# Kernel tuning notes

Measured on AMD Instinct MI355X. Metric: run time of the kernel, lower is better.

Reference implementation:

```python
import jax, jax.numpy as jnp
import numpy as np

T, B, E, H = 2048, 4, 1024, 16
HD = E // H
SCALE = HD ** -0.5


def setup_inputs() -> dict:
    key = jax.random.key(0)
    k1, k2, k3 = jax.random.split(key, 3)
    # xavier-ish scaling on weights for numerical sanity
    inputs = jax.random.normal(k1, (T, B, E), dtype=jnp.float32)
    in_proj_weight = jax.random.normal(k2, (3 * E, E), dtype=jnp.float32) * (2.0 / (4 * E)) ** 0.5
    out_proj_weight = jax.random.normal(k3, (E, E), dtype=jnp.float32) * (1.0 / E) ** 0.5
    return {"inputs": inputs, "in_proj_weight": in_proj_weight, "out_proj_weight": out_proj_weight}


def reference(inputs, in_proj_weight, out_proj_weight):
    t, b, e = inputs.shape
    # fused QKV projection: [T,B,E] @ [E,3E] -> [T, B*H, 3, HD]
    qkv = jnp.einsum('tbe,fe->tbf', inputs, in_proj_weight)
    qkv = qkv.reshape(t, b * H, 3, HD)
    q, k, v = qkv[:, :, 0, :], qkv[:, :, 1, :], qkv[:, :, 2, :]  # [T, B*H, HD]
    # scaled attention scores per (batch*head): [B*H, T, T]
    scores = SCALE * jnp.einsum('tnd,snd->nts', q, k)
    probs = jax.nn.softmax(scores, axis=-1)
    # dropout p=0.0 -> identity
    ctx = jnp.einsum('nts,snd->tnd', probs, v).reshape(t, b, e)
    # output projection (applied to attention context, matching intended math / backward)
    return jnp.einsum('tbe,oe->tbo', ctx, out_proj_weight)
```

## Files before the change

### kernel.cpp

```cpp
#include <hip/hip_runtime.h>
#include <stdint.h>
#include <stddef.h>


typedef __attribute__((ext_vector_type(8))) short bf16x8;
typedef __attribute__((ext_vector_type(4))) float f32x4;
typedef __attribute__((ext_vector_type(4))) unsigned int u32x4;

#define MFMA16(a, b, c) __builtin_amdgcn_mfma_f32_16x16x32_bf16((a), (b), (c), 0, 0, 0)

__device__ __forceinline__ unsigned short f2bf(float f) {
  unsigned u = __builtin_bit_cast(unsigned, f);
  u += 0x7fffu + ((u >> 16) & 1u);
  return (unsigned short)(u >> 16);
}

__device__ __forceinline__ float fast_exp2(float x) {
#if __has_builtin(__builtin_amdgcn_exp2f)
  return __builtin_amdgcn_exp2f(x);
#else
  return exp2f(x);
#endif
}

__device__ __forceinline__ unsigned cvtpk(float lo, float hi) {
  unsigned r;
  asm volatile("v_cvt_pk_bf16_f32 %0, %1, %2" : "=v"(r) : "v"(lo), "v"(hi));
  return r;
}

__device__ __forceinline__ void lane_swap32(unsigned &a, unsigned &b) {
#if __has_builtin(__builtin_amdgcn_permlane32_swap)
  auto r = __builtin_amdgcn_permlane32_swap(a, b, false, false);
  a = r[0]; b = r[1];
#else
  const bool hi = (threadIdx.x & 32) != 0;
  unsigned sa = (unsigned)__shfl_xor((int)a, 32, 64);
  unsigned sb = (unsigned)__shfl_xor((int)b, 32, 64);
  unsigned na = hi ? sb : a;
  unsigned nb = hi ? b : sa;
  a = na; b = nb;
#endif
}

__device__ __forceinline__ void lane_swap16(unsigned &a, unsigned &b) {
  const bool odd = (threadIdx.x & 16) != 0;
  unsigned sa = (unsigned)__shfl_xor((int)a, 16, 64);
  unsigned sb = (unsigned)__shfl_xor((int)b, 16, 64);
  unsigned na = odd ? sb : a;
  unsigned nb = odd ? b : sa;
  a = na; b = nb;
}

__device__ __forceinline__ void gload_lds16(const void* g, void* l) {
  __builtin_amdgcn_global_load_lds((const __attribute__((address_space(1))) void*)g,
                                   (__attribute__((address_space(3))) void*)l,
                                   16, 0, 0);
}

__global__ __launch_bounds__(256) void k_cvt(const float* __restrict__ src,
                                             unsigned short* __restrict__ dst, int n4) {
  int i = blockIdx.x * 256 + threadIdx.x;
  if (i >= n4) return;
  const float4 v = ((const float4*)src)[i];
  ushort4 o;
  o.x = f2bf(v.x); o.y = f2bf(v.y); o.z = f2bf(v.z); o.w = f2bf(v.w);
  ((ushort4*)dst)[i] = o;
}

__global__ __launch_bounds__(256, 2) void k_gemm_qkv(
    const unsigned short* __restrict__ A,
    const unsigned short* __restrict__ Bt,
    unsigned short* __restrict__ Qb,
    unsigned short* __restrict__ Kb,
    unsigned short* __restrict__ VTb) {
  constexpr int K = 1024;
  __shared__ __align__(16) unsigned short As[128 * 32];
  __shared__ __align__(16) unsigned short Bs[128 * 32];
  const int tid = threadIdx.x;
  const int l = tid & 63, w = tid >> 6;
  const int lr = l & 15, lg = l >> 4;
  const int bm = blockIdx.x, bn = blockIdx.y;
  const int wr = (w >> 1) * 64, wc = (w & 1) * 64;

  f32x4 acc[4][4] = {};

  const int o0 = tid * 16, o1 = tid * 16 + 4096;
  const int r0 = o0 >> 6, c0 = o0 & 63;
  const int r1 = o1 >> 6, c1 = o1 & 63;
  const char* gA0 = (const char*)A + (size_t)(bm * 128 + r0) * (K * 2) + c0;
  const char* gA1 = (const char*)A + (size_t)(bm * 128 + r1) * (K * 2) + c1;
  const char* gB0 = (const char*)Bt + (size_t)(bn * 128 + r0) * (K * 2) + c0;
  const char* gB1 = (const char*)Bt + (size_t)(bn * 128 + r1) * (K * 2) + c1;
  char* lA0 = (char*)As + o0;
  char* lA1 = (char*)As + o1;
  char* lB0 = (char*)Bs + o0;
  char* lB1 = (char*)Bs + o1;

  for (int kt = 0; kt < K / 32; ++kt) {
    const int kb = kt * 64;
    gload_lds16(gA0 + kb, lA0);
    gload_lds16(gA1 + kb, lA1);
    gload_lds16(gB0 + kb, lB0);
    gload_lds16(gB1 + kb, lB1);
    __syncthreads();
    bf16x8 af[4], bfr[4];
#pragma unroll
    for (int mf = 0; mf < 4; ++mf)
      af[mf] = *(const bf16x8*)&As[(wr + mf * 16 + lr) * 32 + lg * 8];
#pragma unroll
    for (int nf = 0; nf < 4; ++nf)
      bfr[nf] = *(const bf16x8*)&Bs[(wc + nf * 16 + lr) * 32 + lg * 8];
#pragma unroll
    for (int mf = 0; mf < 4; ++mf)
#pragma unroll
      for (int nf = 0; nf < 4; ++nf)
        acc[mf][nf] = MFMA16(af[mf], bfr[nf], acc[mf][nf]);
    __syncthreads();
  }

#pragma unroll
  for (int nf = 0; nf < 4; ++nf) {
    const int f = bn * 128 + wc + nf * 16 + lr;
    const int hq = f / 192;
    const int s3 = (f >> 6) % 3;
    const int d = f & 63;
    const float qscale = (s3 == 0) ? 0.18033688011112042f : 1.0f;
#pragma unroll
    for (int mf = 0; mf < 4; ++mf) {
#pragma unroll
      for (int i = 0; i < 4; ++i) {
        const int r = bm * 128 + wr + mf * 16 + lg * 4 + i;
        const int t = r >> 2, bb2 = r & 3;
        const int nIdx = bb2 * 16 + hq;
        const unsigned short val = f2bf(acc[mf][nf][i] * qscale);
        if (s3 == 0)      Qb[((size_t)nIdx * 2048 + t) * 64 + d] = val;
        else if (s3 == 1) Kb[((size_t)nIdx * 2048 + t) * 64 + d] = val;
        else              VTb[((size_t)nIdx * 64 + d) * 2048 + t] = val;
      }
    }
  }
}

__global__ __launch_bounds__(256, 2) void k_attn(
    const unsigned short* __restrict__ Qb, const unsigned short* __restrict__ Kb,
    const unsigned short* __restrict__ VTb, unsigned short* __restrict__ Cx) {
  __shared__ __align__(16) unsigned short Ks[64 * 64];
  __shared__ __align__(16) unsigned short Vt[64 * 64];

  const int tid = threadIdx.x;
  const int l = tid & 63, w = tid >> 6;
  const int lq = l & 15, lg = l >> 4;
  const int qt = blockIdx.x, n = blockIdx.y;

  const unsigned short* Qh = Qb + (size_t)n * (2048 * 64);
  const unsigned short* Kh = Kb + (size_t)n * (2048 * 64);
  const unsigned short* Vh = VTb + (size_t)n * (64 * 2048);

  bf16x8 aq[2][2];
#pragma unroll
  for (int qf = 0; qf < 2; ++qf)
#pragma unroll
    for (int kd = 0; kd < 2; ++kd)
      aq[qf][kd] = *(const bf16x8*)&Qh[(size_t)(qt * 128 + w * 32 + qf * 16 + lq) * 64 +
                                       kd * 32 + lg * 8];

  f32x4 o[4][2] = {};
  float lsum[2] = {0.f, 0.f};

#pragma unroll 1
  for (int st = 0; st < 32; ++st) {
    const int s0 = st * 64;
#pragma unroll
    for (int it = 0; it < 2; ++it) {
      const int off = (it * 256 + tid) * 16;
      const int row = off >> 7;
      const int colb = (off & 127) ^ ((row & 7) << 4);
      gload_lds16((const char*)Kh + (size_t)(s0 + row) * 128 + colb, (char*)Ks + off);
      gload_lds16((const char*)Vh + (size_t)row * 4096 + s0 * 2 + colb, (char*)Vt + off);
    }
    __syncthreads();

    f32x4 sc[2][4];
#pragma unroll
    for (int sf = 0; sf < 4; ++sf) {
      const int rowk = sf * 16 + lq;
      const int sw = (rowk & 7) << 4;
      bf16x8 k0 = *(const bf16x8*)((const char*)Ks + ((rowk * 128 + lg * 16) ^ sw));
      bf16x8 k1 = *(const bf16x8*)((const char*)Ks + ((rowk * 128 + 64 + lg * 16) ^ sw));
#pragma unroll
      for (int qf = 0; qf < 2; ++qf) {
        f32x4 z = {0.f, 0.f, 0.f, 0.f};
        z = MFMA16(k0, aq[qf][0], z);
        z = MFMA16(k1, aq[qf][1], z);
        sc[qf][sf] = z;
      }
    }

#pragma unroll
    for (int qf = 0; qf < 2; ++qf) {
      float accs = 0.f;
#pragma unroll
      for (int sf = 0; sf < 4; ++sf)
#pragma unroll
        for (int i = 0; i < 4; ++i) {
          const float p = fast_exp2(sc[qf][sf][i]);
          sc[qf][sf][i] = p;
          accs += p;
        }
      lsum[qf] += accs;
    }

#pragma unroll
    for (int kb = 0; kb < 2; ++kb) {
      bf16x8 pf[2];
#pragma unroll
      for (int qf = 0; qf < 2; ++qf) {
        unsigned w0 = cvtpk(sc[qf][2 * kb + 0][0], sc[qf][2 * kb + 0][1]);
        unsigned w1 = cvtpk(sc[qf][2 * kb + 0][2], sc[qf][2 * kb + 0][3]);
        unsigned w2 = cvtpk(sc[qf][2 * kb + 1][0], sc[qf][2 * kb + 1][1]);
        unsigned w3 = cvtpk(sc[qf][2 * kb + 1][2], sc[qf][2 * kb + 1][3]);
        lane_swap32(w0, w2);
        lane_swap32(w1, w3);
        lane_swap16(w0, w2);
        lane_swap16(w1, w3);
        u32x4 t4 = {w0, w1, w2, w3};
        pf[qf] = __builtin_bit_cast(bf16x8, t4);
      }
#pragma unroll
      for (int df = 0; df < 4; ++df) {
        const int rowd = df * 16 + lq;
        const int sw = (rowd & 7) << 4;
        bf16x8 vf = *(const bf16x8*)((const char*)Vt + ((rowd * 128 + kb * 64 + lg * 16) ^ sw));
#pragma unroll
        for (int qf = 0; qf < 2; ++qf)
          o[df][qf] = MFMA16(vf, pf[qf], o[df][qf]);
      }
    }
    __syncthreads();
  }

  const int bb = n >> 4, h = n & 15;
#pragma unroll
  for (int qf = 0; qf < 2; ++qf) {
    float li = lsum[qf];
    li += __shfl_xor(li, 16, 64);
    li += __shfl_xor(li, 32, 64);
    const float inv = 1.0f / li;
    const int q = qt * 128 + w * 32 + qf * 16 + lq;
#pragma unroll
    for (int df = 0; df < 4; ++df) {
      ushort4 pk;
      pk.x = f2bf(o[df][qf][0] * inv);
      pk.y = f2bf(o[df][qf][1] * inv);
      pk.z = f2bf(o[df][qf][2] * inv);
      pk.w = f2bf(o[df][qf][3] * inv);
      *(ushort4*)&Cx[(size_t)(q * 4 + bb) * 1024 + h * 64 + df * 16 + lg * 4] = pk;
    }
  }
}

__global__ __launch_bounds__(256, 2) void k_gemm_out(
    const unsigned short* __restrict__ A,
    const unsigned short* __restrict__ Bt,
    float* __restrict__ C) {
  constexpr int K = 1024;
  __shared__ __align__(16) unsigned short As[128 * 32];
  __shared__ __align__(16) unsigned short Bs[128 * 32];
  const int tid = threadIdx.x;
  const int l = tid & 63, w = tid >> 6;
  const int lr = l & 15, lg = l >> 4;
  const int bm = blockIdx.x, bn = blockIdx.y;
  const int wr = (w >> 1) * 64, wc = (w & 1) * 64;

  f32x4 acc[4][4] = {};

  const int o0 = tid * 16, o1 = tid * 16 + 4096;
  const int r0 = o0 >> 6, c0 = o0 & 63;
  const int r1 = o1 >> 6, c1 = o1 & 63;
  const char* gA0 = (const char*)A + (size_t)(bm * 128 + r0) * (K * 2) + c0;
  const char* gA1 = (const char*)A + (size_t)(bm * 128 + r1) * (K * 2) + c1;
  const char* gB0 = (const char*)Bt + (size_t)(bn * 128 + r0) * (K * 2) + c0;
  const char* gB1 = (const char*)Bt + (size_t)(bn * 128 + r1) * (K * 2) + c1;
  char* lA0 = (char*)As + o0;
  char* lA1 = (char*)As + o1;
  char* lB0 = (char*)Bs + o0;
  char* lB1 = (char*)Bs + o1;

  for (int kt = 0; kt < K / 32; ++kt) {
    const int kb = kt * 64;
    gload_lds16(gA0 + kb, lA0);
    gload_lds16(gA1 + kb, lA1);
    gload_lds16(gB0 + kb, lB0);
    gload_lds16(gB1 + kb, lB1);
    __syncthreads();
    bf16x8 af[4], bfr[4];
#pragma unroll
    for (int mf = 0; mf < 4; ++mf)
      af[mf] = *(const bf16x8*)&As[(wr + mf * 16 + lr) * 32 + lg * 8];
#pragma unroll
    for (int nf = 0; nf < 4; ++nf)
      bfr[nf] = *(const bf16x8*)&Bs[(wc + nf * 16 + lr) * 32 + lg * 8];
#pragma unroll
    for (int mf = 0; mf < 4; ++mf)
#pragma unroll
      for (int nf = 0; nf < 4; ++nf)
        acc[mf][nf] = MFMA16(af[mf], bfr[nf], acc[mf][nf]);
    __syncthreads();
  }

#pragma unroll
  for (int mf = 0; mf < 4; ++mf)
#pragma unroll
    for (int i = 0; i < 4; ++i) {
      const int r = bm * 128 + wr + mf * 16 + lg * 4 + i;
#pragma unroll
      for (int nf = 0; nf < 4; ++nf)
        C[(size_t)r * 1024 + bn * 128 + wc + nf * 16 + lr] = acc[mf][nf][i];
    }
}

extern "C" void kernel_launch(void* const* d_in, const int* in_sizes, int n_in,
                              void* d_out, int out_size, void* d_ws, size_t ws_size,
                              hipStream_t stream) {
  const float* X = (const float*)d_in[0];
  const float* W1 = (const float*)d_in[1];
  const float* Wo = (const float*)d_in[2];
  float* out = (float*)d_out;

  char* ws = (char*)d_ws;
  unsigned short* Xb  = (unsigned short*)(ws);
  unsigned short* W1b = (unsigned short*)(ws + 16777216);
  unsigned short* Wob = (unsigned short*)(ws + 23068672);
  unsigned short* Qb  = (unsigned short*)(ws + 25165824);
  unsigned short* Kb  = (unsigned short*)(ws + 41943040);
  unsigned short* VTb = (unsigned short*)(ws + 58720256);
  unsigned short* Cx  = (unsigned short*)(ws + 75497472);

  k_cvt<<<8192, 256, 0, stream>>>(X, Xb, 2097152);
  k_cvt<<<3072, 256, 0, stream>>>(W1, W1b, 786432);
  k_cvt<<<1024, 256, 0, stream>>>(Wo, Wob, 262144);
  k_gemm_qkv<<<dim3(64, 24), 256, 0, stream>>>(Xb, W1b, Qb, Kb, VTb);
  k_attn<<<dim3(16, 64), 256, 0, stream>>>(Qb, Kb, VTb, Cx);
  k_gemm_out<<<dim3(64, 8), 256, 0, stream>>>(Cx, Wob, out);
}
```

Measured before the change: 213.2 us.

## Double-buffer attention K/V tiles, add V transpose kernel, use K16 MFMA for PV

Attention now double-buffers the K and V^T LDS tiles, prefetching the next tile while computing the current one, and uses explicit waitcnt and barrier with s_setprio around the MFMA sections. The QKV GEMM writes V in row layout and a new transpose kernel builds V^T, replacing the strided scatter stores. The PV product uses 16x16x16 MFMA when available, which removes the lane-swap permutes. The attention grid is reordered so that blocks sharing a head are adjacent. This adds one kernel launch and an extra V round trip through memory, and it reuses the Cx buffer region for Vb.

```diff
diff --git a/kernel.cpp b/kernel.cpp
--- a/kernel.cpp
+++ b/kernel.cpp
@@ -4,10 +4,17 @@
 
 
 typedef __attribute__((ext_vector_type(8))) short bf16x8;
+typedef __attribute__((ext_vector_type(4))) short bf16x4;
 typedef __attribute__((ext_vector_type(4))) float f32x4;
 typedef __attribute__((ext_vector_type(4))) unsigned int u32x4;
+typedef __attribute__((ext_vector_type(2))) unsigned int u32x2;
 
 #define MFMA16(a, b, c) __builtin_amdgcn_mfma_f32_16x16x32_bf16((a), (b), (c), 0, 0, 0)
+
+#if __has_builtin(__builtin_amdgcn_mfma_f32_16x16x16bf16_1k)
+#define HAVE_K16 1
+#define MFMAK16(a, b, c) __builtin_amdgcn_mfma_f32_16x16x16bf16_1k((a), (b), (c), 0, 0, 0)
+#endif
 
 __device__ __forceinline__ unsigned short f2bf(float f) {
   unsigned u = __builtin_bit_cast(unsigned, f);
@@ -29,6 +36,7 @@
   return r;
 }
 
+#ifndef HAVE_K16
 __device__ __forceinline__ void lane_swap32(unsigned &a, unsigned &b) {
 #if __has_builtin(__builtin_amdgcn_permlane32_swap)
   auto r = __builtin_amdgcn_permlane32_swap(a, b, false, false);
@@ -42,7 +50,6 @@
   a = na; b = nb;
 #endif
 }
-
 __device__ __forceinline__ void lane_swap16(unsigned &a, unsigned &b) {
   const bool odd = (threadIdx.x & 16) != 0;
   unsigned sa = (unsigned)__shfl_xor((int)a, 16, 64);
@@ -51,6 +58,7 @@
   unsigned nb = odd ? b : sa;
   a = na; b = nb;
 }
+#endif
 
 __device__ __forceinline__ void gload_lds16(const void* g, void* l) {
   __builtin_amdgcn_global_load_lds((const __attribute__((address_space(1))) void*)g,
@@ -73,7 +81,7 @@
     const unsigned short* __restrict__ Bt,
     unsigned short* __restrict__ Qb,
     unsigned short* __restrict__ Kb,
-    unsigned short* __restrict__ VTb) {
+    unsigned short* __restrict__ Vb) {
   constexpr int K = 1024;
   __shared__ __align__(16) unsigned short As[128 * 32];
   __shared__ __align__(16) unsigned short Bs[128 * 32];
@@ -125,6 +133,7 @@
     const int hq = f / 192;
     const int s3 = (f >> 6) % 3;
     const int d = f & 63;
+    unsigned short* dst = (s3 == 0) ? Qb : (s3 == 1) ? Kb : Vb;
     const float qscale = (s3 == 0) ? 0.18033688011112042f : 1.0f;
 #pragma unroll
     for (int mf = 0; mf < 4; ++mf) {
@@ -133,25 +142,47 @@
         const int r = bm * 128 + wr + mf * 16 + lg * 4 + i;
         const int t = r >> 2, bb2 = r & 3;
         const int nIdx = bb2 * 16 + hq;
-        const unsigned short val = f2bf(acc[mf][nf][i] * qscale);
-        if (s3 == 0)      Qb[((size_t)nIdx * 2048 + t) * 64 + d] = val;
-        else if (s3 == 1) Kb[((size_t)nIdx * 2048 + t) * 64 + d] = val;
-        else              VTb[((size_t)nIdx * 64 + d) * 2048 + t] = val;
+        dst[((size_t)nIdx * 2048 + t) * 64 + d] = f2bf(acc[mf][nf][i] * qscale);
       }
     }
   }
+}
+
+__global__ __launch_bounds__(256) void k_vtrans(const unsigned short* __restrict__ V,
+                                                unsigned short* __restrict__ VT) {
+  __shared__ unsigned short tile[64][66];
+  const int tid = threadIdx.x;
+  const int n = blockIdx.y, t0 = blockIdx.x * 64;
+  const int r = tid >> 2, c0 = (tid & 3) * 16;
+  const unsigned short* src = V + ((size_t)(n * 2048 + t0 + r) * 64 + c0);
+  bf16x8 a = *(const bf16x8*)src;
+  bf16x8 b = *(const bf16x8*)(src + 8);
+#pragma unroll
+  for (int j = 0; j < 8; ++j) tile[r][c0 + j] = (unsigned short)a[j];
+#pragma unroll
+  for (int j = 0; j < 8; ++j) tile[r][c0 + 8 + j] = (unsigned short)b[j];
+  __syncthreads();
+  const int d = tid >> 2, u0 = (tid & 3) * 16;
+  bf16x8 oA, oB;
+#pragma unroll
+  for (int j = 0; j < 8; ++j) oA[j] = (short)tile[u0 + j][d];
+#pragma unroll
+  for (int j = 0; j < 8; ++j) oB[j] = (short)tile[u0 + 8 + j][d];
+  unsigned short* dst = VT + ((size_t)(n * 64 + d) * 2048 + t0 + u0);
+  *(bf16x8*)dst = oA;
+  *(bf16x8*)(dst + 8) = oB;
 }
 
 __global__ __launch_bounds__(256, 2) void k_attn(
     const unsigned short* __restrict__ Qb, const unsigned short* __restrict__ Kb,
     const unsigned short* __restrict__ VTb, unsigned short* __restrict__ Cx) {
-  __shared__ __align__(16) unsigned short Ks[64 * 64];
-  __shared__ __align__(16) unsigned short Vt[64 * 64];
+  __shared__ __align__(16) unsigned short Ks[2][64 * 64];
+  __shared__ __align__(16) unsigned short Vt[2][64 * 64];
 
   const int tid = threadIdx.x;
   const int l = tid & 63, w = tid >> 6;
   const int lq = l & 15, lg = l >> 4;
-  const int qt = blockIdx.x, n = blockIdx.y;
+  const int n = blockIdx.x, qt = blockIdx.y;
 
   const unsigned short* Qh = Qb + (size_t)n * (2048 * 64);
   const unsigned short* Kh = Kb + (size_t)n * (2048 * 64);
@@ -168,26 +199,41 @@
   f32x4 o[4][2] = {};
   float lsum[2] = {0.f, 0.f};
 
-#pragma unroll 1
-  for (int st = 0; st < 32; ++st) {
+  char* Ksl = (char*)&Ks[0][0];
+  char* Vtl = (char*)&Vt[0][0];
+
+  auto STAGE = [&](int buf, int st) {
     const int s0 = st * 64;
 #pragma unroll
     for (int it = 0; it < 2; ++it) {
       const int off = (it * 256 + tid) * 16;
       const int row = off >> 7;
       const int colb = (off & 127) ^ ((row & 7) << 4);
-      gload_lds16((const char*)Kh + (size_t)(s0 + row) * 128 + colb, (char*)Ks + off);
-      gload_lds16((const char*)Vh + (size_t)row * 4096 + s0 * 2 + colb, (char*)Vt + off);
-    }
-    __syncthreads();
+      gload_lds16((const char*)Kh + ((size_t)(s0 + row) << 7) + colb, Ksl + buf * 8192 + off);
+      gload_lds16((const char*)Vh + ((size_t)row << 12) + (s0 << 1) + colb, Vtl + buf * 8192 + off);
+    }
+  };
+
+  STAGE(0, 0);
+  asm volatile("s_waitcnt vmcnt(0)" ::: "memory");
+  __builtin_amdgcn_s_barrier();
+
+#pragma unroll 2
+  for (int st = 0; st < 32; ++st) {
+    const int cur = st & 1;
+    if (st + 1 < 32) STAGE(cur ^ 1, st + 1);
+
+    const char* Kc = Ksl + cur * 8192;
+    const char* Vc = Vtl + cur * 8192;
 
     f32x4 sc[2][4];
+    __builtin_amdgcn_s_setprio(1);
 #pragma unroll
     for (int sf = 0; sf < 4; ++sf) {
       const int rowk = sf * 16 + lq;
       const int sw = (rowk & 7) << 4;
-      bf16x8 k0 = *(const bf16x8*)((const char*)Ks + ((rowk * 128 + lg * 16) ^ sw));
-      bf16x8 k1 = *(const bf16x8*)((const char*)Ks + ((rowk * 128 + 64 + lg * 16) ^ sw));
+      bf16x8 k0 = *(const bf16x8*)(Kc + ((rowk * 128 + lg * 16) ^ sw));
+      bf16x8 k1 = *(const bf16x8*)(Kc + ((rowk * 128 + 64 + lg * 16) ^ sw));
 #pragma unroll
       for (int qf = 0; qf < 2; ++qf) {
         f32x4 z = {0.f, 0.f, 0.f, 0.f};
@@ -196,6 +242,7 @@
         sc[qf][sf] = z;
       }
     }
+    __builtin_amdgcn_s_setprio(0);
 
 #pragma unroll
     for (int qf = 0; qf < 2; ++qf) {
@@ -211,6 +258,27 @@
       lsum[qf] += accs;
     }
 
+    __builtin_amdgcn_s_setprio(1);
+#ifdef HAVE_K16
+#pragma unroll
+    for (int sf = 0; sf < 4; ++sf) {
+      bf16x4 pf[2];
+#pragma unroll
+      for (int qf = 0; qf < 2; ++qf) {
+        u32x2 pu = {cvtpk(sc[qf][sf][0], sc[qf][sf][1]),
+                    cvtpk(sc[qf][sf][2], sc[qf][sf][3])};
+        pf[qf] = __builtin_bit_cast(bf16x4, pu);
+      }
+#pragma unroll
+      for (int df = 0; df < 4; ++df) {
+        const int rowd = df * 16 + lq;
+        const int sw = (rowd & 7) << 4;
+        bf16x4 vf = *(const bf16x4*)(Vc + ((rowd * 128 + sf * 32 + lg * 8) ^ sw));
+        o[df][0] = MFMAK16(vf, pf[0], o[df][0]);
+        o[df][1] = MFMAK16(vf, pf[1], o[df][1]);
+      }
+    }
+#else
 #pragma unroll
     for (int kb = 0; kb < 2; ++kb) {
       bf16x8 pf[2];
@@ -231,13 +299,17 @@
       for (int df = 0; df < 4; ++df) {
         const int rowd = df * 16 + lq;
         const int sw = (rowd & 7) << 4;
-        bf16x8 vf = *(const bf16x8*)((const char*)Vt + ((rowd * 128 + kb * 64 + lg * 16) ^ sw));
+        bf16x8 vf = *(const bf16x8*)(Vc + ((rowd * 128 + kb * 64 + lg * 16) ^ sw));
 #pragma unroll
         for (int qf = 0; qf < 2; ++qf)
           o[df][qf] = MFMA16(vf, pf[qf], o[df][qf]);
       }
     }
-    __syncthreads();
+#endif
+    __builtin_amdgcn_s_setprio(0);
+
+    asm volatile("s_waitcnt vmcnt(0)" ::: "memory");
+    __builtin_amdgcn_s_barrier();
   }
 
   const int bb = n >> 4, h = n & 15;
@@ -335,12 +407,14 @@
   unsigned short* Qb  = (unsigned short*)(ws + 25165824);
   unsigned short* Kb  = (unsigned short*)(ws + 41943040);
   unsigned short* VTb = (unsigned short*)(ws + 58720256);
+  unsigned short* Vb  = (unsigned short*)(ws + 75497472);
   unsigned short* Cx  = (unsigned short*)(ws + 75497472);
 
   k_cvt<<<8192, 256, 0, stream>>>(X, Xb, 2097152);
   k_cvt<<<3072, 256, 0, stream>>>(W1, W1b, 786432);
   k_cvt<<<1024, 256, 0, stream>>>(Wo, Wob, 262144);
-  k_gemm_qkv<<<dim3(64, 24), 256, 0, stream>>>(Xb, W1b, Qb, Kb, VTb);
-  k_attn<<<dim3(16, 64), 256, 0, stream>>>(Qb, Kb, VTb, Cx);
+  k_gemm_qkv<<<dim3(64, 24), 256, 0, stream>>>(Xb, W1b, Qb, Kb, Vb);
+  k_vtrans<<<dim3(32, 64), 256, 0, stream>>>(Vb, VTb);
+  k_attn<<<dim3(64, 16), 256, 0, stream>>>(Qb, Kb, VTb, Cx);
   k_gemm_out<<<dim3(64, 8), 256, 0, stream>>>(Cx, Wob, out);
 }
```

New measurement: 212.1 us. Within noise of the previous version (-0.5%).
